# Optimization experiments

Measured on AMD Instinct MI355X. Metric: run time of the kernel, lower is better.

## Reference

```python
import jax, jax.numpy as jnp
import numpy as np

B, N, D = 8, 2048, 128
NHID = 256
PROJ = 64            # Wq/Wk output dim
THETA_IN = D + NHID + 3   # 387
THETA_HID = 128
ALPHA = 0.2
TAU = 1.0
CLUSTER_SIZE_MAX = 3


def setup_inputs() -> dict:
    key = jax.random.key(0)
    ks = jax.random.split(key, 12)
    x = jax.random.normal(ks[0], (B, N, D), dtype=jnp.float32)
    adj = (jax.random.uniform(ks[1], (B, N, N)) < 0.01).astype(jnp.float32)
    # current cluster membership: a handful of nodes per graph
    cluster_mask = (jax.random.uniform(ks[2], (B, N)) < 0.002).astype(jnp.float32)
    cand_mask = (jax.random.uniform(ks[3], (B, N)) < 0.3).astype(jnp.float32)
    seed_ctx_feats = jax.random.normal(ks[4], (B, D + NHID), dtype=jnp.float32)
    local_stats = jax.random.uniform(ks[5], (B, 3), dtype=jnp.float32)
    # parameters
    Wq = jax.random.normal(ks[6], (PROJ, D), dtype=jnp.float32) / np.sqrt(D)
    Wk = jax.random.normal(ks[7], (PROJ, D), dtype=jnp.float32) / np.sqrt(D)
    W1 = jax.random.normal(ks[8], (THETA_IN, THETA_HID), dtype=jnp.float32) / np.sqrt(THETA_IN)
    b1 = jnp.zeros((THETA_HID,), dtype=jnp.float32)
    W2 = jax.random.normal(ks[9], (THETA_HID, 1), dtype=jnp.float32) / np.sqrt(THETA_HID)
    b2 = jnp.zeros((1,), dtype=jnp.float32)
    return {"x": x, "adj": adj, "seed_ctx_feats": seed_ctx_feats,
            "local_stats": local_stats, "cluster_mask": cluster_mask,
            "cand_mask": cand_mask, "Wq": Wq, "Wk": Wk,
            "W1": W1, "b1": b1, "W2": W2, "b2": b2}


def reference(x, adj, seed_ctx_feats, local_stats, cluster_mask, cand_mask,
              Wq, Wk, W1, b1, W2, b2):
    b, n, _ = x.shape
    # key projections and seed query (seed = argmax of cluster mask)
    x_k = jnp.einsum('bnd,hd->bnh', x, Wk)                       # [B,N,64]
    seed_idx = jnp.argmax(cluster_mask, axis=-1)                 # [B]
    seed_x = x[jnp.arange(b), seed_idx]                          # [B,D]
    q = jnp.einsum('bd,hd->bh', seed_x, Wq)                      # [B,64]
    scores = jnp.einsum('bnh,bh->bn', x_k, q) / jnp.sqrt(jnp.float32(PROJ))
    # edges-to-cluster term, degree-normalized
    e2c = jnp.einsum('bnm,bm->bn', adj, cluster_mask)            # [B,N]
    deg = jnp.maximum(jnp.sum(adj, axis=-1), 1.0)                # [B,N]
    cand_scores = scores + ALPHA * (e2c / deg)
    # threshold head: Linear -> ReLU -> Linear
    theta_in = jnp.concatenate([seed_ctx_feats, local_stats], axis=-1)
    h = jax.nn.relu(theta_in @ W1 + b1)
    theta = (h @ W2 + b2)[..., 0]                                # [B]
    # sigmoid gate
    logits = (cand_scores - theta[:, None]) / max(TAU, 1e-6)
    p = jax.nn.sigmoid(logits) * cand_mask
    # top-k cap (k_cap = cluster_size_max - 1), applied only where over cap
    k_cap = CLUSTER_SIZE_MAX - 1
    over = jnp.sum((p > 0.5).astype(p.dtype), axis=-1) - k_cap   # [B], no grad (bool cmp)
    need_trim = over > 0
    _, topk_idx = jax.lax.top_k(p, max(k_cap, 1))                # [B,k]
    keep = jnp.zeros_like(p).at[jnp.arange(b)[:, None], topk_idx].set(1.0)
    p = jnp.where(need_trim[:, None], p * keep, p)
    # straight-through hard gate
    hard = (p > 0.5).astype(p.dtype) + (p - jax.lax.stop_gradient(p))
    return hard, p, theta
```

## Files before the change

kernel.cpp:

```cpp
#include <hip/hip_runtime.h>
#include <math.h>

#define NB 8
#define NN 2048
#define ND 128
#define NHID 256
#define PROJ 64
#define TH_IN 387
#define TH_HID 128

__global__ __launch_bounds__(1024) void seed_theta_kernel(
    const float* __restrict__ x, const float* __restrict__ seed_ctx,
    const float* __restrict__ local_stats, const float* __restrict__ cmask,
    const float* __restrict__ Wq, const float* __restrict__ Wk,
    const float* __restrict__ W1, const float* __restrict__ b1,
    const float* __restrict__ W2, const float* __restrict__ b2,
    float* __restrict__ kq_ws, float* __restrict__ theta_ws,
    int* __restrict__ cidx, float* __restrict__ cval, int* __restrict__ ccnt,
    float* __restrict__ out_theta)
{
  const int b = blockIdx.x;
  const int t = threadIdx.x;
  const int wave = t >> 6, lane = t & 63;

  __shared__ float swv[16]; __shared__ int swi[16];
  __shared__ float sx[ND];
  __shared__ float sq[PROJ];
  __shared__ float tin[TH_IN];
  __shared__ float part[8][TH_HID];
  __shared__ float sred[TH_HID];
  __shared__ int s_seed, s_cnt;

  if (t == 0) s_cnt = 0;

  const float c0 = cmask[b*NN + t];
  const float c1 = cmask[b*NN + t + 1024];
  {
    float bv = c0; int bi = t;
    if (c1 > bv) { bv = c1; bi = t + 1024; }
    for (int off = 32; off; off >>= 1) {
      float ov = __shfl_xor(bv, off);
      int   oi = __shfl_xor(bi, off);
      if (ov > bv || (ov == bv && oi < bi)) { bv = ov; bi = oi; }
    }
    if (lane == 0) { swv[wave] = bv; swi[wave] = bi; }
  }
  __syncthreads();

  if (c0 != 0.f) { int s = atomicAdd(&s_cnt, 1); cidx[b*NN+s] = t;        cval[b*NN+s] = c0; }
  if (c1 != 0.f) { int s = atomicAdd(&s_cnt, 1); cidx[b*NN+s] = t + 1024; cval[b*NN+s] = c1; }

  if (t == 0) {
    float bv = swv[0]; int bi = swi[0];
    #pragma unroll
    for (int w = 1; w < 16; ++w)
      if (swv[w] > bv || (swv[w] == bv && swi[w] < bi)) { bv = swv[w]; bi = swi[w]; }
    s_seed = bi;
  }
  __syncthreads();
  if (t == 0) ccnt[b] = s_cnt;
  const int seed = s_seed;

  if (t < ND) sx[t] = x[((size_t)b*NN + seed)*ND + t];
  __syncthreads();

  {
    const int h = wave*4;
    #pragma unroll
    for (int j = 0; j < 4; ++j) {
      float a = Wq[(h+j)*ND + lane] * sx[lane]
              + Wq[(h+j)*ND + 64 + lane] * sx[64 + lane];
      for (int off = 32; off; off >>= 1) a += __shfl_xor(a, off);
      if (lane == 0) sq[h+j] = a;
    }
  }
  __syncthreads();

  {
    const int c = t >> 7;
    const int d = t & 127;
    float acc = 0.f;
    #pragma unroll
    for (int j = 0; j < 8; ++j) acc += Wk[(c*8 + j)*ND + d] * sq[c*8 + j];
    part[c][d] = acc;
  }
  __syncthreads();
  if (t < ND) {
    float acc = 0.f;
    #pragma unroll
    for (int c = 0; c < 8; ++c) acc += part[c][t];
    kq_ws[b*ND + t] = acc;
  }

  if (t < ND + NHID) tin[t] = seed_ctx[b*(ND+NHID) + t];
  if (t >= ND + NHID && t < TH_IN) tin[t] = local_stats[b*3 + (t - (ND+NHID))];
  __syncthreads();
  {
    const int c = t >> 7;
    const int h = t & 127;
    const int i0 = c*49;
    const int i1 = (c == 7) ? TH_IN : i0 + 49;
    float acc = 0.f;
    for (int i = i0; i < i1; ++i) acc += tin[i] * W1[i*TH_HID + h];
    part[c][h] = acc;
  }
  __syncthreads();
  if (t < TH_HID) {
    float acc = b1[t];
    #pragma unroll
    for (int c = 0; c < 8; ++c) acc += part[c][t];
    acc = fmaxf(acc, 0.f);
    sred[t] = acc * W2[t];
  }
  __syncthreads();
  if (t < 64) {
    float v = sred[t] + sred[t + 64];
    for (int off = 32; off; off >>= 1) v += __shfl_xor(v, off);
    if (t == 0) {
      float th = v + b2[0];
      theta_ws[b] = th;
      out_theta[b] = th;
    }
  }
}

__global__ __launch_bounds__(512) void row_kernel(
    const float* __restrict__ x, const float* __restrict__ adj,
    const float* __restrict__ candm,
    const float* __restrict__ kq_ws, const float* __restrict__ theta_ws,
    const int* __restrict__ cidx, const float* __restrict__ cval,
    const int* __restrict__ ccnt,
    float* __restrict__ out_hard, float* __restrict__ out_p,
    float* __restrict__ pv1, int* __restrict__ pi1,
    float* __restrict__ pv2, int* __restrict__ pi2, int* __restrict__ pcnt)
{
  const int t = threadIdx.x;
  const int wave = t >> 6, lane = t & 63;
  const int row0 = blockIdx.x * 8;
  const int b = row0 >> 11;
  __shared__ float sKq[ND];
  __shared__ float sTheta; __shared__ int sK;
  __shared__ float rv[8]; __shared__ int rc[8];

  if (t < ND) sKq[t] = kq_ws[b*ND + t];
  if (t == 0) { sTheta = theta_ws[b]; sK = ccnt[b]; }
  __syncthreads();
  const int K = sK;

  const int row = row0 + wave;
  const float cm = candm[row];

  float p = 0.f;
  if (cm != 0.f) {
    const float* arow = adj + (size_t)row * NN;

    const float2* x2 = (const float2*)(x + (size_t)row * ND);
    float2 xv = x2[lane];
    float sc = xv.x * sKq[2*lane] + xv.y * sKq[2*lane + 1];

    float e2c = 0.f;
    if (lane < K) e2c = arow[cidx[b*NN + lane]] * cval[b*NN + lane];
    for (int base = 64; base < K; base += 64) {
      const int k = base + lane;
      if (k < K) e2c += arow[cidx[b*NN + k]] * cval[b*NN + k];
    }

    for (int off = 32; off; off >>= 1) {
      sc  += __shfl_xor(sc, off);
      e2c += __shfl_xor(e2c, off);
    }

    float extra = 0.f;
    if (e2c != 0.f) {
      const float4* a4 = (const float4*)arow;
      float deg = 0.f;
      #pragma unroll
      for (int k = 0; k < 8; ++k) {
        float4 a = a4[k*64 + lane];
        deg += a.x + a.y + a.z + a.w;
      }
      for (int off = 32; off; off >>= 1) deg += __shfl_xor(deg, off);
      extra = e2c / fmaxf(deg, 1.0f);
    }

    float cand = sc * 0.125f + 0.2f * extra;
    p = (1.0f / (1.0f + expf(-(cand - sTheta)))) * cm;
  }

  if (lane == 0) {
    out_p[row] = p;
    out_hard[row] = (p > 0.5f) ? 1.0f : 0.0f;
    rv[wave] = p; rc[wave] = (p > 0.5f) ? 1 : 0;
  }
  __syncthreads();
  if (t == 0) {
    float V1 = -1e30f, V2 = -1e30f; int I1 = 0, I2 = 0, cnt = 0;
    #pragma unroll
    for (int w = 0; w < 8; ++w) {
      float v = rv[w]; int idx = (row0 & (NN-1)) + w;
      cnt += rc[w];
      if (v > V1)      { V2=V1; I2=I1; V1=v; I1=idx; }
      else if (v > V2) { V2=v;  I2=idx; }
    }
    pv1[blockIdx.x] = V1; pi1[blockIdx.x] = I1;
    pv2[blockIdx.x] = V2; pi2[blockIdx.x] = I2;
    pcnt[blockIdx.x] = cnt;
  }
}

__global__ __launch_bounds__(256) void trim_kernel(
    const float* __restrict__ pv1, const int* __restrict__ pi1,
    const float* __restrict__ pv2, const int* __restrict__ pi2,
    const int* __restrict__ pcnt,
    float* __restrict__ out_hard, float* __restrict__ out_p)
{
  const int b = blockIdx.x;
  const int t = threadIdx.x;
  const int g = b*256 + t;
  __shared__ int scnt[256];
  __shared__ float sv1[256]; __shared__ int si1[256];
  __shared__ float sv2[256]; __shared__ int si2[256];
  __shared__ int s_trim, s_k1, s_k2;

  scnt[t] = pcnt[g];
  sv1[t] = pv1[g]; si1[t] = pi1[g];
  sv2[t] = pv2[g]; si2[t] = pi2[g];
  __syncthreads();
  for (int s = 128; s > 0; s >>= 1) {
    if (t < s) {
      scnt[t] += scnt[t+s];
      float B1 = sv1[t+s]; int Bi1 = si1[t+s];
      float B2 = sv2[t+s]; int Bi2 = si2[t+s];
      float V1 = sv1[t], V2 = sv2[t]; int I1 = si1[t], I2 = si2[t];
      if (B1 > V1)      { V2=V1; I2=I1; V1=B1; I1=Bi1; }
      else if (B1 > V2) { V2=B1; I2=Bi1; }
      if (B2 > V1)      { V2=V1; I2=I1; V1=B2; I1=Bi2; }
      else if (B2 > V2) { V2=B2; I2=Bi2; }
      sv1[t]=V1; si1[t]=I1; sv2[t]=V2; si2[t]=I2;
    }
    __syncthreads();
  }
  if (t == 0) {
    s_trim = (scnt[0] > 2) ? 1 : 0;
    s_k1 = si1[0]; s_k2 = si2[0];
  }
  __syncthreads();
  if (s_trim) {
    float* p    = out_p    + b*NN;
    float* hard = out_hard + b*NN;
    #pragma unroll
    for (int j = 0; j < 8; ++j) {
      const int nidx = j*256 + t;
      if (nidx != s_k1 && nidx != s_k2) { p[nidx] = 0.f; hard[nidx] = 0.f; }
    }
  }
}

extern "C" void kernel_launch(void* const* d_in, const int* in_sizes, int n_in,
                              void* d_out, int out_size, void* d_ws, size_t ws_size,
                              hipStream_t stream) {
  const float* x          = (const float*)d_in[0];
  const float* adj        = (const float*)d_in[1];
  const float* seed_ctx   = (const float*)d_in[2];
  const float* local_st   = (const float*)d_in[3];
  const float* cmask      = (const float*)d_in[4];
  const float* candm      = (const float*)d_in[5];
  const float* Wq         = (const float*)d_in[6];
  const float* Wk         = (const float*)d_in[7];
  const float* W1         = (const float*)d_in[8];
  const float* b1         = (const float*)d_in[9];
  const float* W2         = (const float*)d_in[10];
  const float* b2         = (const float*)d_in[11];

  float* out      = (float*)d_out;
  float* out_hard = out;
  float* out_p    = out + NB*NN;
  float* out_th   = out + 2*NB*NN;

  const int NBLK = NB*NN/8;
  float* ws       = (float*)d_ws;
  float* kq_ws    = ws;
  float* theta_ws = ws + NB*ND;
  float* pv1      = ws + NB*ND + NB;
  float* pv2      = pv1 + NBLK;
  int*   pi1      = (int*)(pv2 + NBLK);
  int*   pi2      = pi1 + NBLK;
  int*   pcnt     = pi2 + NBLK;
  int*   cidx     = pcnt + NBLK;
  float* cval     = (float*)(cidx + NB*NN);
  int*   ccnt     = (int*)(cval + NB*NN);

  seed_theta_kernel<<<NB, 1024, 0, stream>>>(x, seed_ctx, local_st, cmask,
                                             Wq, Wk, W1, b1, W2, b2,
                                             kq_ws, theta_ws,
                                             cidx, cval, ccnt, out_th);
  row_kernel<<<NBLK, 512, 0, stream>>>(x, adj, candm, kq_ws, theta_ws,
                                       cidx, cval, ccnt,
                                       out_hard, out_p, pv1, pi1, pv2, pi2, pcnt);
  trim_kernel<<<NB, 256, 0, stream>>>(pv1, pi1, pv2, pi2, pcnt,
                                      out_hard, out_p);
}
```

Before: 27.33 us.

## Split seed and theta head into parallel blocks; skip row blocks without candidates

The per-batch seed/theta kernel now launches two 512-thread blocks per batch. One finds the seed and cluster list and computes the Wk·q vector; the other computes the threshold MLP, so the two serial chains run concurrently. The row kernel loads the eight candidate mask values first and exits early, writing zeros and empty partial top-k entries, when none of its rows is a candidate. The early exit rarely fires at the given candidate density and adds an extra barrier to every row block.

```diff
diff --git a/kernel.cpp b/kernel.cpp
--- a/kernel.cpp
+++ b/kernel.cpp
@@ -9,7 +9,7 @@
 #define TH_IN 387
 #define TH_HID 128
 
-__global__ __launch_bounds__(1024) void seed_theta_kernel(
+__global__ __launch_bounds__(512) void seed_theta_kernel(
     const float* __restrict__ x, const float* __restrict__ seed_ctx,
     const float* __restrict__ local_stats, const float* __restrict__ cmask,
     const float* __restrict__ Wq, const float* __restrict__ Wk,
@@ -19,107 +19,111 @@
     int* __restrict__ cidx, float* __restrict__ cval, int* __restrict__ ccnt,
     float* __restrict__ out_theta)
 {
-  const int b = blockIdx.x;
+  const int b = blockIdx.x >> 1;
+  const int path = blockIdx.x & 1;
   const int t = threadIdx.x;
   const int wave = t >> 6, lane = t & 63;
 
-  __shared__ float swv[16]; __shared__ int swi[16];
-  __shared__ float sx[ND];
-  __shared__ float sq[PROJ];
-  __shared__ float tin[TH_IN];
-  __shared__ float part[8][TH_HID];
-  __shared__ float sred[TH_HID];
-  __shared__ int s_seed, s_cnt;
-
-  if (t == 0) s_cnt = 0;
-
-  const float c0 = cmask[b*NN + t];
-  const float c1 = cmask[b*NN + t + 1024];
-  {
-    float bv = c0; int bi = t;
-    if (c1 > bv) { bv = c1; bi = t + 1024; }
-    for (int off = 32; off; off >>= 1) {
-      float ov = __shfl_xor(bv, off);
-      int   oi = __shfl_xor(bi, off);
-      if (ov > bv || (ov == bv && oi < bi)) { bv = ov; bi = oi; }
-    }
-    if (lane == 0) { swv[wave] = bv; swi[wave] = bi; }
-  }
-  __syncthreads();
-
-  if (c0 != 0.f) { int s = atomicAdd(&s_cnt, 1); cidx[b*NN+s] = t;        cval[b*NN+s] = c0; }
-  if (c1 != 0.f) { int s = atomicAdd(&s_cnt, 1); cidx[b*NN+s] = t + 1024; cval[b*NN+s] = c1; }
-
-  if (t == 0) {
-    float bv = swv[0]; int bi = swi[0];
-    #pragma unroll
-    for (int w = 1; w < 16; ++w)
-      if (swv[w] > bv || (swv[w] == bv && swi[w] < bi)) { bv = swv[w]; bi = swi[w]; }
-    s_seed = bi;
-  }
-  __syncthreads();
-  if (t == 0) ccnt[b] = s_cnt;
-  const int seed = s_seed;
-
-  if (t < ND) sx[t] = x[((size_t)b*NN + seed)*ND + t];
-  __syncthreads();
-
-  {
-    const int h = wave*4;
-    #pragma unroll
-    for (int j = 0; j < 4; ++j) {
-      float a = Wq[(h+j)*ND + lane] * sx[lane]
-              + Wq[(h+j)*ND + 64 + lane] * sx[64 + lane];
-      for (int off = 32; off; off >>= 1) a += __shfl_xor(a, off);
-      if (lane == 0) sq[h+j] = a;
-    }
-  }
-  __syncthreads();
-
-  {
-    const int c = t >> 7;
-    const int d = t & 127;
-    float acc = 0.f;
-    #pragma unroll
-    for (int j = 0; j < 8; ++j) acc += Wk[(c*8 + j)*ND + d] * sq[c*8 + j];
-    part[c][d] = acc;
-  }
-  __syncthreads();
-  if (t < ND) {
-    float acc = 0.f;
-    #pragma unroll
-    for (int c = 0; c < 8; ++c) acc += part[c][t];
-    kq_ws[b*ND + t] = acc;
-  }
-
-  if (t < ND + NHID) tin[t] = seed_ctx[b*(ND+NHID) + t];
-  if (t >= ND + NHID && t < TH_IN) tin[t] = local_stats[b*3 + (t - (ND+NHID))];
-  __syncthreads();
-  {
-    const int c = t >> 7;
-    const int h = t & 127;
-    const int i0 = c*49;
-    const int i1 = (c == 7) ? TH_IN : i0 + 49;
-    float acc = 0.f;
-    for (int i = i0; i < i1; ++i) acc += tin[i] * W1[i*TH_HID + h];
-    part[c][h] = acc;
-  }
-  __syncthreads();
-  if (t < TH_HID) {
-    float acc = b1[t];
-    #pragma unroll
-    for (int c = 0; c < 8; ++c) acc += part[c][t];
-    acc = fmaxf(acc, 0.f);
-    sred[t] = acc * W2[t];
-  }
-  __syncthreads();
-  if (t < 64) {
-    float v = sred[t] + sred[t + 64];
-    for (int off = 32; off; off >>= 1) v += __shfl_xor(v, off);
+  if (path == 0) {
+    __shared__ float swv[8]; __shared__ int swi[8];
+    __shared__ float sx[ND];
+    __shared__ float sq[PROJ];
+    __shared__ float part[4][ND];
+    __shared__ int s_seed, s_cnt;
+
+    if (t == 0) s_cnt = 0;
+
+    const float c0 = cmask[b*NN + t];
+    const float c1 = cmask[b*NN + t + 512];
+    const float c2 = cmask[b*NN + t + 1024];
+    const float c3 = cmask[b*NN + t + 1536];
+    {
+      float bv = c0; int bi = t;
+      if (c1 > bv) { bv = c1; bi = t + 512; }
+      if (c2 > bv) { bv = c2; bi = t + 1024; }
+      if (c3 > bv) { bv = c3; bi = t + 1536; }
+      for (int off = 32; off; off >>= 1) {
+        float ov = __shfl_xor(bv, off);
+        int   oi = __shfl_xor(bi, off);
+        if (ov > bv || (ov == bv && oi < bi)) { bv = ov; bi = oi; }
+      }
+      if (lane == 0) { swv[wave] = bv; swi[wave] = bi; }
+    }
+    __syncthreads();
+
+    if (c0 != 0.f) { int s = atomicAdd(&s_cnt,1); cidx[b*NN+s] = t;        cval[b*NN+s] = c0; }
+    if (c1 != 0.f) { int s = atomicAdd(&s_cnt,1); cidx[b*NN+s] = t + 512;  cval[b*NN+s] = c1; }
+    if (c2 != 0.f) { int s = atomicAdd(&s_cnt,1); cidx[b*NN+s] = t + 1024; cval[b*NN+s] = c2; }
+    if (c3 != 0.f) { int s = atomicAdd(&s_cnt,1); cidx[b*NN+s] = t + 1536; cval[b*NN+s] = c3; }
+
     if (t == 0) {
-      float th = v + b2[0];
-      theta_ws[b] = th;
-      out_theta[b] = th;
+      float bv = swv[0]; int bi = swi[0];
+      #pragma unroll
+      for (int w = 1; w < 8; ++w)
+        if (swv[w] > bv || (swv[w] == bv && swi[w] < bi)) { bv = swv[w]; bi = swi[w]; }
+      s_seed = bi;
+    }
+    __syncthreads();
+    if (t == 0) ccnt[b] = s_cnt;
+    const int seed = s_seed;
+
+    if (t < ND) sx[t] = x[((size_t)b*NN + seed)*ND + t];
+    __syncthreads();
+
+    {
+      const int h0 = wave*8;
+      #pragma unroll
+      for (int j = 0; j < 8; ++j) {
+        float a = Wq[(h0+j)*ND + lane] * sx[lane]
+                + Wq[(h0+j)*ND + 64 + lane] * sx[64 + lane];
+        for (int off = 32; off; off >>= 1) a += __shfl_xor(a, off);
+        if (lane == 0) sq[h0+j] = a;
+      }
+    }
+    __syncthreads();
+
+    {
+      const int hc = t >> 7, d = t & 127;
+      float acc = 0.f;
+      #pragma unroll
+      for (int j = 0; j < 16; ++j) acc += Wk[(hc*16 + j)*ND + d] * sq[hc*16 + j];
+      part[hc][d] = acc;
+    }
+    __syncthreads();
+    if (t < ND) kq_ws[b*ND + t] = part[0][t] + part[1][t] + part[2][t] + part[3][t];
+
+  } else {
+    __shared__ float tin[TH_IN];
+    __shared__ float part[4][TH_HID];
+    __shared__ float sred[TH_HID];
+
+    if (t < TH_IN)
+      tin[t] = (t < ND + NHID) ? seed_ctx[b*(ND+NHID) + t]
+                               : local_stats[b*3 + (t - (ND+NHID))];
+    __syncthreads();
+    {
+      const int c = t >> 7, h = t & 127;
+      const int i0 = c*97;
+      const int i1 = (c == 3) ? TH_IN : i0 + 97;
+      float acc = 0.f;
+      for (int i = i0; i < i1; ++i) acc += tin[i] * W1[i*TH_HID + h];
+      part[c][h] = acc;
+    }
+    __syncthreads();
+    if (t < TH_HID) {
+      float acc = b1[t] + part[0][t] + part[1][t] + part[2][t] + part[3][t];
+      acc = fmaxf(acc, 0.f);
+      sred[t] = acc * W2[t];
+    }
+    __syncthreads();
+    if (t < 64) {
+      float v = sred[t] + sred[t + 64];
+      for (int off = 32; off; off >>= 1) v += __shfl_xor(v, off);
+      if (t == 0) {
+        float th = v + b2[0];
+        theta_ws[b] = th;
+        out_theta[b] = th;
+      }
     }
   }
 }
@@ -140,15 +144,31 @@
   const int b = row0 >> 11;
   __shared__ float sKq[ND];
   __shared__ float sTheta; __shared__ int sK;
+  __shared__ float scm[8];
   __shared__ float rv[8]; __shared__ int rc[8];
 
+  if (t < 8) scm[t] = candm[row0 + t];
+  if (t == 0) { sTheta = theta_ws[b]; sK = ccnt[b]; }
+  __syncthreads();
+
+  const bool anyc = (scm[0]!=0.f)|(scm[1]!=0.f)|(scm[2]!=0.f)|(scm[3]!=0.f)|
+                    (scm[4]!=0.f)|(scm[5]!=0.f)|(scm[6]!=0.f)|(scm[7]!=0.f);
+  if (!anyc) {
+    if (t < 8) { out_p[row0+t] = 0.f; out_hard[row0+t] = 0.f; }
+    if (t == 0) {
+      pv1[blockIdx.x] = -1e30f; pi1[blockIdx.x] = 0;
+      pv2[blockIdx.x] = -1e30f; pi2[blockIdx.x] = 0;
+      pcnt[blockIdx.x] = 0;
+    }
+    return;
+  }
+
   if (t < ND) sKq[t] = kq_ws[b*ND + t];
-  if (t == 0) { sTheta = theta_ws[b]; sK = ccnt[b]; }
   __syncthreads();
   const int K = sK;
 
   const int row = row0 + wave;
-  const float cm = candm[row];
+  const float cm = scm[wave];
 
   float p = 0.f;
   if (cm != 0.f) {
@@ -290,10 +310,10 @@
   float* cval     = (float*)(cidx + NB*NN);
   int*   ccnt     = (int*)(cval + NB*NN);
 
-  seed_theta_kernel<<<NB, 1024, 0, stream>>>(x, seed_ctx, local_st, cmask,
-                                             Wq, Wk, W1, b1, W2, b2,
-                                             kq_ws, theta_ws,
-                                             cidx, cval, ccnt, out_th);
+  seed_theta_kernel<<<2*NB, 512, 0, stream>>>(x, seed_ctx, local_st, cmask,
+                                              Wq, Wk, W1, b1, W2, b2,
+                                              kq_ws, theta_ws,
+                                              cidx, cval, ccnt, out_th);
   row_kernel<<<NBLK, 512, 0, stream>>>(x, adj, candm, kq_ws, theta_ws,
                                        cidx, cval, ccnt,
                                        out_hard, out_p, pv1, pi1, pv2, pi2, pcnt);
```

Result: no change. 27.60 us (+1.0%).
